# Kernel tuning notes

Measured on AMD Instinct MI355X. Metric: run time of the kernel, lower is better.

Reference implementation:

```python
import jax, jax.numpy as jnp
import numpy as np

D = 1024        # d_hidden
DE = 512        # d_expert (routed)
E = 8           # n_routed_experts
TOP_K = 2
DS = DE * 2     # shared expert width = d_expert * n_shared_experts


def setup_inputs() -> dict:
    key = jax.random.key(0)
    ks = jax.random.split(key, 8)
    s = 1.0 / np.sqrt(D)
    return {
        "x": jax.random.normal(ks[0], (2, 1024, D), dtype=jnp.float32),
        "W_g": jax.random.normal(ks[1], (D, E), dtype=jnp.float32) * s,
        "Wg_e": jax.random.normal(ks[2], (E, D, DE), dtype=jnp.float32) * s,
        "Wu_e": jax.random.normal(ks[3], (E, D, DE), dtype=jnp.float32) * s,
        "Wd_e": jax.random.normal(ks[4], (E, DE, D), dtype=jnp.float32) * (1.0 / np.sqrt(DE)),
        "Wg_s": jax.random.normal(ks[5], (D, DS), dtype=jnp.float32) * s,
        "Wu_s": jax.random.normal(ks[6], (D, DS), dtype=jnp.float32) * s,
        "Wd_s": jax.random.normal(ks[7], (DS, D), dtype=jnp.float32) * (1.0 / np.sqrt(DS)),
    }


def _moe(x, W_g, Wg_e, Wu_e, Wd_e, Wg_s, Wu_s, Wd_s):
    B, T, Dm = x.shape
    N = B * T
    xf = x.reshape(N, Dm)

    # shared expert (SwiGLU)
    shared = (jax.nn.silu(xf @ Wg_s) * (xf @ Wu_s)) @ Wd_s  # [N, D]

    # gating: softmax then top-k (set membership identical to torch sorted=False)
    probs = jax.nn.softmax(xf @ W_g, axis=-1)               # [N, E]
    topk_vals, topk_ids = jax.lax.top_k(probs, TOP_K)       # [N, K]

    # combine weights c[n, e] = sum of topk_vals where routed to expert e
    # (equivalent to the original gather -> weighted scatter_add combine)
    c = jnp.zeros((N, E), dtype=x.dtype)
    c = c.at[jnp.arange(N)[:, None], topk_ids].add(topk_vals)

    # dense per-expert SwiGLU, weighted-combined (same math as gather/scatter loop)
    gate = jax.nn.silu(jnp.einsum('nd,edh->neh', xf, Wg_e))
    up = jnp.einsum('nd,edh->neh', xf, Wu_e)
    routed = jnp.einsum('neh,ne,ehd->nd', gate * up, c, Wd_e)  # [N, D]

    return (shared + routed).reshape(B, T, Dm)


def reference(x, W_g, Wg_e, Wu_e, Wd_e, Wg_s, Wu_s, Wd_s):
    return _moe(x, W_g, Wg_e, Wu_e, Wd_e, Wg_s, Wu_s, Wd_s)
```

## Files before the change

### kernel.cpp

```cpp
#include <hip/hip_runtime.h>
#include <hip/hip_bf16.h>

#define NTOK 2048
#define DIM  1024
#define DEXP 512
#define NEXP 8
#define DSH  1024
#define KH   5120
#define MAXROWS 5120

typedef __hip_bfloat16 bf16;
typedef __attribute__((ext_vector_type(8))) short bf16x8;
typedef __attribute__((ext_vector_type(4))) float floatx4;

__device__ __forceinline__ void gl_lds16(const bf16* g, bf16* l) {
    __builtin_amdgcn_global_load_lds(
        (const __attribute__((address_space(1))) void*)g,
        (__attribute__((address_space(3))) void*)l, 16, 0, 0);
}

__device__ __forceinline__ float b2f(short s) {
    union { float f; unsigned u; } v;
    v.u = ((unsigned)(unsigned short)s) << 16;
    return v.f;
}

__global__ __launch_bounds__(256) void cast_x_kernel(const float* __restrict__ src,
                                                     bf16* __restrict__ dst, int n4) {
    int i = blockIdx.x * 256 + threadIdx.x;
    if (i >= n4) return;
    float4 v = ((const float4*)src)[i];
    struct B4 { bf16 a, b, c, d; };
    B4 o{__float2bfloat16(v.x), __float2bfloat16(v.y),
         __float2bfloat16(v.z), __float2bfloat16(v.w)};
    ((B4*)dst)[i] = o;
}

__global__ __launch_bounds__(256) void pack_weights(
        const float* __restrict__ Wg_s, const float* __restrict__ Wu_s,
        const float* __restrict__ Wg_e, const float* __restrict__ Wu_e,
        const float* __restrict__ Wd_s, const float* __restrict__ Wd_e,
        bf16* __restrict__ Bg, bf16* __restrict__ Bu, bf16* __restrict__ Bd) {
    __shared__ float t[32][33];
    int b = blockIdx.x;
    const float* src; bf16* dst; int C; long dstStride, dstBase; int tilesX;
    if (b < 1024)       { src = Wg_s; dst = Bg; C = 1024; dstStride = 1024; dstBase = 0; tilesX = 32; }
    else if (b < 2048)  { b -= 1024; src = Wu_s; dst = Bu; C = 1024; dstStride = 1024; dstBase = 0; tilesX = 32; }
    else if (b < 6144)  { b -= 2048; int z = b >> 9; b &= 511;
                          src = Wg_e + (long)z * DIM * DEXP; dst = Bg; C = 512;
                          dstStride = 1024; dstBase = (long)(DSH + z * DEXP) * 1024; tilesX = 16; }
    else if (b < 10240) { b -= 6144; int z = b >> 9; b &= 511;
                          src = Wu_e + (long)z * DIM * DEXP; dst = Bu; C = 512;
                          dstStride = 1024; dstBase = (long)(DSH + z * DEXP) * 1024; tilesX = 16; }
    else if (b < 11264) { b -= 10240; src = Wd_s; dst = Bd; C = 1024; dstStride = KH; dstBase = 0; tilesX = 32; }
    else                { b -= 11264; int z = b >> 9; b &= 511;
                          src = Wd_e + (long)z * DEXP * DIM; dst = Bd; C = 1024;
                          dstStride = KH; dstBase = DSH + (long)z * DEXP; tilesX = 32; }
    int tileX = b & (tilesX - 1), tileY = b / tilesX;
    int c0 = tileX * 32, r0 = tileY * 32;
    int tx = threadIdx.x & 31, ty = threadIdx.x >> 5;
#pragma unroll
    for (int i = 0; i < 4; i++)
        t[ty + i * 8][tx] = src[(long)(r0 + ty + i * 8) * C + c0 + tx];
    __syncthreads();
#pragma unroll
    for (int i = 0; i < 4; i++)
        dst[dstBase + (long)(c0 + ty + i * 8) * dstStride + r0 + tx] =
            __float2bfloat16(t[tx][ty + i * 8]);
}

__global__ __launch_bounds__(256) void gate_kernel(const float* __restrict__ x,
                                                   const float* __restrict__ Wg,
                                                   int* __restrict__ counts,
                                                   int* __restrict__ tok_list,
                                                   float* __restrict__ cw,
                                                   int4* __restrict__ tok2slot) {
    int t = blockIdx.x * 4 + (threadIdx.x >> 6);
    int lane = threadIdx.x & 63;
    float acc[NEXP] = {0.f, 0.f, 0.f, 0.f, 0.f, 0.f, 0.f, 0.f};
    const float* xr = x + (long)t * DIM;
    for (int d = lane; d < DIM; d += 64) {
        float xv = xr[d];
        float4 w0 = *(const float4*)(Wg + d * NEXP);
        float4 w1 = *(const float4*)(Wg + d * NEXP + 4);
        acc[0] += xv * w0.x; acc[1] += xv * w0.y; acc[2] += xv * w0.z; acc[3] += xv * w0.w;
        acc[4] += xv * w1.x; acc[5] += xv * w1.y; acc[6] += xv * w1.z; acc[7] += xv * w1.w;
    }
#pragma unroll
    for (int e = 0; e < NEXP; e++)
#pragma unroll
        for (int off = 32; off; off >>= 1)
            acc[e] += __shfl_xor(acc[e], off);
    if (lane == 0) {
        float m = acc[0];
#pragma unroll
        for (int e = 1; e < NEXP; e++) m = fmaxf(m, acc[e]);
        float p[NEXP], s = 0.f;
#pragma unroll
        for (int e = 0; e < NEXP; e++) { p[e] = expf(acc[e] - m); s += p[e]; }
        float inv = 1.f / s;
#pragma unroll
        for (int e = 0; e < NEXP; e++) p[e] *= inv;
        int i1 = 0;
#pragma unroll
        for (int e = 1; e < NEXP; e++) if (p[e] > p[i1]) i1 = e;
        int i2 = (i1 == 0) ? 1 : 0;
#pragma unroll
        for (int e = 0; e < NEXP; e++) if (e != i1 && p[e] > p[i2]) i2 = e;
        int s1 = atomicAdd(counts + i1, 1);
        tok_list[i1 * NTOK + s1] = t;
        cw[i1 * NTOK + s1] = p[i1];
        int s2 = atomicAdd(counts + i2, 1);
        tok_list[i2 * NTOK + s2] = t;
        cw[i2 * NTOK + s2] = p[i2];
        tok2slot[t] = make_int4(i1, s1, i2, s2);
    }
}

__global__ void scan_kernel(const int* __restrict__ counts, int* __restrict__ offs) {
    if (threadIdx.x == 0) {
        int o = 0;
#pragma unroll
        for (int e = 0; e < NEXP; e++) { offs[e] = o; o += (counts[e] + 127) & ~127; }
    }
}

__global__ __launch_bounds__(256) void gu_all(const bf16* __restrict__ X,
                                              const bf16* __restrict__ Bg,
                                              const bf16* __restrict__ Bu,
                                              const int* __restrict__ counts,
                                              const int* __restrict__ offs,
                                              const int* __restrict__ tok_list,
                                              const float* __restrict__ cw,
                                              bf16* __restrict__ Hs,
                                              bf16* __restrict__ He) {
    __shared__ __align__(16) bf16 sA[128 * 32];
    __shared__ __align__(16) bf16 sBg[64 * 32];
    __shared__ __align__(16) bf16 sBu[64 * 32];

    const int b = blockIdx.x;
    const bool routed = b < 1024;
    int e = 0, m, c;
    if (routed) {
        e = b >> 7; m = (b >> 3) & 15; c = b & 7;
        if (m * 128 >= counts[e]) return;
    } else {
        int bs = b - 1024; m = bs >> 4; c = bs & 15;
    }
    const int so = routed ? offs[e] : 0;
    const int colB0 = routed ? (DSH + e * DEXP + c * 64) : c * 64;

    const int tid = threadIdx.x;
    const int wave = tid >> 6, lane = tid & 63;
    const int wr = wave >> 1, wc = wave & 1;
    const int q = lane >> 4, l15 = lane & 15;
    const int koff = (q ^ ((l15 >> 1) & 3)) * 8;

    const int r0 = tid >> 2, c4 = tid & 3;
    const int r1 = r0 + 64;
    const int c4s = c4 ^ ((r0 >> 1) & 3);
    long aRow0, aRow1;
    if (routed) {
        const int* tl = tok_list + e * NTOK + m * 128;
        aRow0 = (long)tl[r0] * DIM;
        aRow1 = (long)tl[r1] * DIM;
    } else {
        aRow0 = (long)(m * 128 + r0) * DIM;
        aRow1 = (long)(m * 128 + r1) * DIM;
    }
    const long bRow = (long)(colB0 + r0) * DIM;

    floatx4 accG[4][2], accU[4][2];
    const floatx4 z4 = {0.f, 0.f, 0.f, 0.f};
#pragma unroll
    for (int i = 0; i < 4; i++)
#pragma unroll
        for (int j = 0; j < 2; j++) { accG[i][j] = z4; accU[i][j] = z4; }

    for (int k0 = 0; k0 < DIM; k0 += 32) {
        gl_lds16(X + aRow0 + k0 + c4s * 8, sA + (wave * 64) * 8);
        gl_lds16(X + aRow1 + k0 + c4s * 8, sA + (256 + wave * 64) * 8);
        gl_lds16(Bg + bRow + k0 + c4s * 8, sBg + (wave * 64) * 8);
        gl_lds16(Bu + bRow + k0 + c4s * 8, sBu + (wave * 64) * 8);
        __syncthreads();

        bf16x8 af[4], bg[2], bu[2];
#pragma unroll
        for (int rt = 0; rt < 4; rt++)
            af[rt] = *(const bf16x8*)(sA + (wr * 64 + rt * 16 + l15) * 32 + koff);
#pragma unroll
        for (int ct = 0; ct < 2; ct++) {
            int cb = (wc * 32 + ct * 16 + l15) * 32 + koff;
            bg[ct] = *(const bf16x8*)(sBg + cb);
            bu[ct] = *(const bf16x8*)(sBu + cb);
        }
#pragma unroll
        for (int rt = 0; rt < 4; rt++)
#pragma unroll
            for (int ct = 0; ct < 2; ct++) {
                accG[rt][ct] = __builtin_amdgcn_mfma_f32_16x16x32_bf16(af[rt], bg[ct], accG[rt][ct], 0, 0, 0);
                accU[rt][ct] = __builtin_amdgcn_mfma_f32_16x16x32_bf16(af[rt], bu[ct], accU[rt][ct], 0, 0, 0);
            }
        __syncthreads();
    }

    float wv[4][4];
#pragma unroll
    for (int rt = 0; rt < 4; rt++)
#pragma unroll
        for (int r = 0; r < 4; r++) {
            int srow = wr * 64 + rt * 16 + q * 4 + r;
            wv[rt][r] = routed ? cw[e * NTOK + m * 128 + srow] : 1.0f;
        }
#pragma unroll
    for (int rt = 0; rt < 4; rt++)
#pragma unroll
        for (int ct = 0; ct < 2; ct++)
#pragma unroll
            for (int r = 0; r < 4; r++) {
                int srow = wr * 64 + rt * 16 + q * 4 + r;
                int colLoc = c * 64 + wc * 32 + ct * 16 + l15;
                float g = accG[rt][ct][r];
                float u = accU[rt][ct][r];
                float h = (g / (1.f + __expf(-g))) * u * wv[rt][r];
                if (routed)
                    He[(long)(so + m * 128 + srow) * DEXP + colLoc] = __float2bfloat16(h);
                else
                    Hs[(long)(m * 128 + srow) * DSH + colLoc] = __float2bfloat16(h);
            }
}

__global__ __launch_bounds__(256) void down_all(const bf16* __restrict__ Hs,
                                                const bf16* __restrict__ He,
                                                const bf16* __restrict__ Bd,
                                                const int* __restrict__ counts,
                                                const int* __restrict__ offs,
                                                bf16* __restrict__ Ys,
                                                bf16* __restrict__ Ye) {
    __shared__ __align__(16) bf16 sA[128 * 32];
    __shared__ __align__(16) bf16 sB[64 * 32];

    const int b = blockIdx.x;
    const bool routed = b < 2048;
    int e = 0, m, cc;
    if (routed) {
        e = b >> 8; m = (b >> 4) & 15; cc = b & 15;
        if (m * 128 >= counts[e]) return;
    } else {
        int bs = b - 2048; m = bs >> 4; cc = bs & 15;
    }
    const int so = routed ? offs[e] : 0;
    const bf16* A = routed ? He + (long)so * DEXP : Hs;
    bf16* Y = routed ? Ye + (long)so * DIM : Ys;
    const int astr = routed ? DEXP : DSH;
    const int ksteps = routed ? (DEXP / 32) : (DSH / 32);
    const int kg0 = routed ? (DSH + e * DEXP) : 0;

    const int tid = threadIdx.x;
    const int wave = tid >> 6, lane = tid & 63;
    const int wr = wave >> 1, wc = wave & 1;
    const int q = lane >> 4, l15 = lane & 15;
    const int koff = (q ^ ((l15 >> 1) & 3)) * 8;

    const int r0 = tid >> 2, c4 = tid & 3;
    const int r1 = r0 + 64;
    const int c4s = c4 ^ ((r0 >> 1) & 3);
    const long aRow0 = (long)(m * 128 + r0) * astr;
    const long aRow1 = (long)(m * 128 + r1) * astr;
    const long bRow = (long)(cc * 64 + r0) * KH + kg0;

    floatx4 acc[4][2];
    const floatx4 z4 = {0.f, 0.f, 0.f, 0.f};
#pragma unroll
    for (int i = 0; i < 4; i++)
#pragma unroll
        for (int j = 0; j < 2; j++) acc[i][j] = z4;

    for (int ks = 0; ks < ksteps; ks++) {
        const int k0 = ks * 32;
        gl_lds16(A + aRow0 + k0 + c4s * 8, sA + (wave * 64) * 8);
        gl_lds16(A + aRow1 + k0 + c4s * 8, sA + (256 + wave * 64) * 8);
        gl_lds16(Bd + bRow + k0 + c4s * 8, sB + (wave * 64) * 8);
        __syncthreads();

        bf16x8 af[4], bb[2];
#pragma unroll
        for (int rt = 0; rt < 4; rt++)
            af[rt] = *(const bf16x8*)(sA + (wr * 64 + rt * 16 + l15) * 32 + koff);
#pragma unroll
        for (int ct = 0; ct < 2; ct++)
            bb[ct] = *(const bf16x8*)(sB + (wc * 32 + ct * 16 + l15) * 32 + koff);
#pragma unroll
        for (int rt = 0; rt < 4; rt++)
#pragma unroll
            for (int ct = 0; ct < 2; ct++)
                acc[rt][ct] = __builtin_amdgcn_mfma_f32_16x16x32_bf16(af[rt], bb[ct], acc[rt][ct], 0, 0, 0);
        __syncthreads();
    }

#pragma unroll
    for (int rt = 0; rt < 4; rt++)
#pragma unroll
        for (int ct = 0; ct < 2; ct++)
#pragma unroll
            for (int r = 0; r < 4; r++) {
                int srow = wr * 64 + rt * 16 + q * 4 + r;
                int mc = cc * 64 + wc * 32 + ct * 16 + l15;
                Y[(long)(m * 128 + srow) * DIM + mc] = __float2bfloat16(acc[rt][ct][r]);
            }
}

__global__ __launch_bounds__(256) void combine_kernel(const bf16* __restrict__ Ys,
                                                      const bf16* __restrict__ Ye,
                                                      const int4* __restrict__ t2s,
                                                      const int* __restrict__ offs,
                                                      float* __restrict__ out) {
    int idx = blockIdx.x * 256 + threadIdx.x;
    int t = idx >> 7;
    int d = (idx & 127) * 8;
    int4 ts = t2s[t];
    bf16x8 a = *(const bf16x8*)(Ys + (long)t * DIM + d);
    bf16x8 p = *(const bf16x8*)(Ye + ((long)offs[ts.x] + ts.y) * DIM + d);
    bf16x8 r = *(const bf16x8*)(Ye + ((long)offs[ts.z] + ts.w) * DIM + d);
    float* o = out + (long)t * DIM + d;
#pragma unroll
    for (int i = 0; i < 8; i++)
        o[i] = b2f(a[i]) + b2f(p[i]) + b2f(r[i]);
}

extern "C" void kernel_launch(void* const* d_in, const int* in_sizes, int n_in,
                              void* d_out, int out_size, void* d_ws, size_t ws_size,
                              hipStream_t stream) {
    const float* x    = (const float*)d_in[0];
    const float* W_g  = (const float*)d_in[1];
    const float* Wg_e = (const float*)d_in[2];
    const float* Wu_e = (const float*)d_in[3];
    const float* Wd_e = (const float*)d_in[4];
    const float* Wd_s_dummy = nullptr; (void)Wd_s_dummy;
    const float* Wg_s = (const float*)d_in[5];
    const float* Wu_s = (const float*)d_in[6];
    const float* Wd_s = (const float*)d_in[7];
    float* out = (float*)d_out;

    bf16* Xb = (bf16*)d_ws;
    bf16* Bg = Xb + (size_t)NTOK * DIM;
    bf16* Bu = Bg + (size_t)KH * DIM;
    bf16* Bd = Bu + (size_t)KH * DIM;
    bf16* Hs = Bd + (size_t)DIM * KH;
    bf16* He = Hs + (size_t)NTOK * DSH;
    bf16* Ys = He + (size_t)MAXROWS * DEXP;
    bf16* Ye = Ys + (size_t)NTOK * DIM;
    int*  counts   = (int*)(Ye + (size_t)MAXROWS * DIM);
    int*  offs     = counts + NEXP;
    int*  tok_list = offs + NEXP;
    float* cw      = (float*)(tok_list + NEXP * NTOK);
    int4* tok2slot = (int4*)(cw + NEXP * NTOK);
    const size_t metaBytes = sizeof(int) * 2 * NEXP
                           + sizeof(int) * NEXP * NTOK + sizeof(float) * NEXP * NTOK;

    hipMemsetAsync(counts, 0, metaBytes, stream);
    cast_x_kernel<<<(NTOK * DIM / 4 + 255) / 256, 256, 0, stream>>>(x, Xb, NTOK * DIM / 4);
    pack_weights<<<15360, 256, 0, stream>>>(Wg_s, Wu_s, Wg_e, Wu_e, Wd_s, Wd_e, Bg, Bu, Bd);
    gate_kernel<<<NTOK / 4, 256, 0, stream>>>(x, W_g, counts, tok_list, cw, tok2slot);
    scan_kernel<<<1, 64, 0, stream>>>(counts, offs);
    gu_all<<<1280, 256, 0, stream>>>(Xb, Bg, Bu, counts, offs, tok_list, cw, Hs, He);
    down_all<<<2304, 256, 0, stream>>>(Hs, He, Bd, counts, offs, Ys, Ye);
    combine_kernel<<<NTOK * DIM / 8 / 256, 256, 0, stream>>>(Ys, Ye, tok2slot, offs, out);
}
```

Before: 238.2 us.

## Fuse x cast into gating, replace atomics with deterministic ballot assignment, vectorize weight pack

The bf16 cast of x now happens inside the gating-logits kernel, so x is read once instead of twice. Slot assignment moves from per-token atomics to a single-block ballot/popcount pass that also computes the padded offsets, which removes the separate scan kernel and makes routing order deterministic. The weight-pack transpose now uses float4 loads and 4-wide bf16 stores with a padded LDS tile. The single-block assign kernel serializes 2048 tokens across 8 waves and adds a launch, though both costs are small.

```diff
diff --git a/kernel.cpp b/kernel.cpp
--- a/kernel.cpp
+++ b/kernel.cpp
@@ -25,15 +25,99 @@
     return v.f;
 }
 
-__global__ __launch_bounds__(256) void cast_x_kernel(const float* __restrict__ src,
-                                                     bf16* __restrict__ dst, int n4) {
-    int i = blockIdx.x * 256 + threadIdx.x;
-    if (i >= n4) return;
-    float4 v = ((const float4*)src)[i];
-    struct B4 { bf16 a, b, c, d; };
-    B4 o{__float2bfloat16(v.x), __float2bfloat16(v.y),
-         __float2bfloat16(v.z), __float2bfloat16(v.w)};
-    ((B4*)dst)[i] = o;
+struct B4 { bf16 a, b, c, d; };
+
+__global__ __launch_bounds__(256) void gate_logits(const float* __restrict__ x,
+                                                   const float* __restrict__ Wg,
+                                                   bf16* __restrict__ Xb,
+                                                   int2* __restrict__ te,
+                                                   float2* __restrict__ tp) {
+    int t = blockIdx.x * 4 + (threadIdx.x >> 6);
+    int lane = threadIdx.x & 63;
+    const float* xr = x + (long)t * DIM;
+    bf16* xo = Xb + (long)t * DIM;
+    float acc[NEXP] = {0.f, 0.f, 0.f, 0.f, 0.f, 0.f, 0.f, 0.f};
+#pragma unroll
+    for (int i = 0; i < 4; i++) {
+        int d = lane * 4 + i * 256;
+        float4 xv = *(const float4*)(xr + d);
+        B4 o{__float2bfloat16(xv.x), __float2bfloat16(xv.y),
+             __float2bfloat16(xv.z), __float2bfloat16(xv.w)};
+        *(B4*)(xo + d) = o;
+#pragma unroll
+        for (int j = 0; j < 4; j++) {
+            float xs = (j == 0) ? xv.x : (j == 1) ? xv.y : (j == 2) ? xv.z : xv.w;
+            float4 w0 = *(const float4*)(Wg + (d + j) * NEXP);
+            float4 w1 = *(const float4*)(Wg + (d + j) * NEXP + 4);
+            acc[0] += xs * w0.x; acc[1] += xs * w0.y; acc[2] += xs * w0.z; acc[3] += xs * w0.w;
+            acc[4] += xs * w1.x; acc[5] += xs * w1.y; acc[6] += xs * w1.z; acc[7] += xs * w1.w;
+        }
+    }
+#pragma unroll
+    for (int e = 0; e < NEXP; e++)
+#pragma unroll
+        for (int off = 32; off; off >>= 1)
+            acc[e] += __shfl_xor(acc[e], off);
+    if (lane == 0) {
+        float m = acc[0];
+#pragma unroll
+        for (int e = 1; e < NEXP; e++) m = fmaxf(m, acc[e]);
+        float p[NEXP], s = 0.f;
+#pragma unroll
+        for (int e = 0; e < NEXP; e++) { p[e] = expf(acc[e] - m); s += p[e]; }
+        float inv = 1.f / s;
+#pragma unroll
+        for (int e = 0; e < NEXP; e++) p[e] *= inv;
+        int i1 = 0;
+#pragma unroll
+        for (int e = 1; e < NEXP; e++) if (p[e] > p[i1]) i1 = e;
+        int i2 = (i1 == 0) ? 1 : 0;
+#pragma unroll
+        for (int e = 0; e < NEXP; e++) if (e != i1 && p[e] > p[i2]) i2 = e;
+        te[t] = make_int2(i1, i2);
+        tp[t] = make_float2(p[i1], p[i2]);
+    }
+}
+
+__global__ __launch_bounds__(512) void assign_kernel(const int2* __restrict__ te,
+                                                     const float2* __restrict__ tp,
+                                                     int* __restrict__ counts,
+                                                     int* __restrict__ offs,
+                                                     int* __restrict__ tok_list,
+                                                     float* __restrict__ cw,
+                                                     int* __restrict__ s1a,
+                                                     int* __restrict__ s2a) {
+    __shared__ int cnt[NEXP];
+    const int e = threadIdx.x >> 6;
+    const int lane = threadIdx.x & 63;
+    int base = 0;
+    for (int t0 = 0; t0 < NTOK; t0 += 64) {
+        int t = t0 + lane;
+        int2 ee = te[t];
+        bool m1 = (ee.x == e), m2 = (ee.y == e);
+        bool mt = m1 || m2;
+        unsigned long long mask = __ballot(mt);
+        int pre = __popcll(mask & ((1ull << lane) - 1ull));
+        if (mt) {
+            int slot = base + pre;
+            tok_list[e * NTOK + slot] = t;
+            float2 pp = tp[t];
+            cw[e * NTOK + slot] = m1 ? pp.x : pp.y;
+            if (m1) s1a[t] = slot; else s2a[t] = slot;
+        }
+        base += __popcll(mask);
+    }
+    if (lane == 0) cnt[e] = base;
+    __syncthreads();
+    if (threadIdx.x == 0) {
+        int o = 0;
+#pragma unroll
+        for (int i = 0; i < NEXP; i++) {
+            counts[i] = cnt[i];
+            offs[i] = o;
+            o += (cnt[i] + 127) & ~127;
+        }
+    }
 }
 
 __global__ __launch_bounds__(256) void pack_weights(
@@ -41,7 +125,7 @@
         const float* __restrict__ Wg_e, const float* __restrict__ Wu_e,
         const float* __restrict__ Wd_s, const float* __restrict__ Wd_e,
         bf16* __restrict__ Bg, bf16* __restrict__ Bu, bf16* __restrict__ Bd) {
-    __shared__ float t[32][33];
+    __shared__ float t[32][36];
     int b = blockIdx.x;
     const float* src; bf16* dst; int C; long dstStride, dstBase; int tilesX;
     if (b < 1024)       { src = Wg_s; dst = Bg; C = 1024; dstStride = 1024; dstBase = 0; tilesX = 32; }
@@ -58,70 +142,19 @@
                           dstStride = KH; dstBase = DSH + (long)z * DEXP; tilesX = 32; }
     int tileX = b & (tilesX - 1), tileY = b / tilesX;
     int c0 = tileX * 32, r0 = tileY * 32;
-    int tx = threadIdx.x & 31, ty = threadIdx.x >> 5;
-#pragma unroll
-    for (int i = 0; i < 4; i++)
-        t[ty + i * 8][tx] = src[(long)(r0 + ty + i * 8) * C + c0 + tx];
+
+    {
+        int row = threadIdx.x >> 3, ch = threadIdx.x & 7;
+        float4 v = *(const float4*)(src + (long)(r0 + row) * C + c0 + ch * 4);
+        *(float4*)(&t[row][ch * 4]) = v;
+    }
     __syncthreads();
-#pragma unroll
-    for (int i = 0; i < 4; i++)
-        dst[dstBase + (long)(c0 + ty + i * 8) * dstStride + r0 + tx] =
-            __float2bfloat16(t[tx][ty + i * 8]);
-}
-
-__global__ __launch_bounds__(256) void gate_kernel(const float* __restrict__ x,
-                                                   const float* __restrict__ Wg,
-                                                   int* __restrict__ counts,
-                                                   int* __restrict__ tok_list,
-                                                   float* __restrict__ cw,
-                                                   int4* __restrict__ tok2slot) {
-    int t = blockIdx.x * 4 + (threadIdx.x >> 6);
-    int lane = threadIdx.x & 63;
-    float acc[NEXP] = {0.f, 0.f, 0.f, 0.f, 0.f, 0.f, 0.f, 0.f};
-    const float* xr = x + (long)t * DIM;
-    for (int d = lane; d < DIM; d += 64) {
-        float xv = xr[d];
-        float4 w0 = *(const float4*)(Wg + d * NEXP);
-        float4 w1 = *(const float4*)(Wg + d * NEXP + 4);
-        acc[0] += xv * w0.x; acc[1] += xv * w0.y; acc[2] += xv * w0.z; acc[3] += xv * w0.w;
-        acc[4] += xv * w1.x; acc[5] += xv * w1.y; acc[6] += xv * w1.z; acc[7] += xv * w1.w;
-    }
-#pragma unroll
-    for (int e = 0; e < NEXP; e++)
-#pragma unroll
-        for (int off = 32; off; off >>= 1)
-            acc[e] += __shfl_xor(acc[e], off);
-    if (lane == 0) {
-        float m = acc[0];
-#pragma unroll
-        for (int e = 1; e < NEXP; e++) m = fmaxf(m, acc[e]);
-        float p[NEXP], s = 0.f;
-#pragma unroll
-        for (int e = 0; e < NEXP; e++) { p[e] = expf(acc[e] - m); s += p[e]; }
-        float inv = 1.f / s;
-#pragma unroll
-        for (int e = 0; e < NEXP; e++) p[e] *= inv;
-        int i1 = 0;
-#pragma unroll
-        for (int e = 1; e < NEXP; e++) if (p[e] > p[i1]) i1 = e;
-        int i2 = (i1 == 0) ? 1 : 0;
-#pragma unroll
-        for (int e = 0; e < NEXP; e++) if (e != i1 && p[e] > p[i2]) i2 = e;
-        int s1 = atomicAdd(counts + i1, 1);
-        tok_list[i1 * NTOK + s1] = t;
-        cw[i1 * NTOK + s1] = p[i1];
-        int s2 = atomicAdd(counts + i2, 1);
-        tok_list[i2 * NTOK + s2] = t;
-        cw[i2 * NTOK + s2] = p[i2];
-        tok2slot[t] = make_int4(i1, s1, i2, s2);
-    }
-}
-
-__global__ void scan_kernel(const int* __restrict__ counts, int* __restrict__ offs) {
-    if (threadIdx.x == 0) {
-        int o = 0;
-#pragma unroll
-        for (int e = 0; e < NEXP; e++) { offs[e] = o; o += (counts[e] + 127) & ~127; }
+    {
+        int dc = threadIdx.x & 31, ch = threadIdx.x >> 5;
+        int j = ch * 4;
+        B4 o{__float2bfloat16(t[j][dc]), __float2bfloat16(t[j + 1][dc]),
+             __float2bfloat16(t[j + 2][dc]), __float2bfloat16(t[j + 3][dc])};
+        *(B4*)(dst + dstBase + (long)(c0 + dc) * dstStride + r0 + j) = o;
     }
 }
 
@@ -312,16 +345,20 @@
 
 __global__ __launch_bounds__(256) void combine_kernel(const bf16* __restrict__ Ys,
                                                       const bf16* __restrict__ Ye,
-                                                      const int4* __restrict__ t2s,
+                                                      const int2* __restrict__ te,
+                                                      const int* __restrict__ s1a,
+                                                      const int* __restrict__ s2a,
                                                       const int* __restrict__ offs,
                                                       float* __restrict__ out) {
     int idx = blockIdx.x * 256 + threadIdx.x;
     int t = idx >> 7;
     int d = (idx & 127) * 8;
-    int4 ts = t2s[t];
+    int2 ee = te[t];
+    long r1 = (long)(offs[ee.x] + s1a[t]);
+    long r2 = (long)(offs[ee.y] + s2a[t]);
     bf16x8 a = *(const bf16x8*)(Ys + (long)t * DIM + d);
-    bf16x8 p = *(const bf16x8*)(Ye + ((long)offs[ts.x] + ts.y) * DIM + d);
-    bf16x8 r = *(const bf16x8*)(Ye + ((long)offs[ts.z] + ts.w) * DIM + d);
+    bf16x8 p = *(const bf16x8*)(Ye + r1 * DIM + d);
+    bf16x8 r = *(const bf16x8*)(Ye + r2 * DIM + d);
     float* o = out + (long)t * DIM + d;
 #pragma unroll
     for (int i = 0; i < 8; i++)
@@ -336,7 +373,6 @@
     const float* Wg_e = (const float*)d_in[2];
     const float* Wu_e = (const float*)d_in[3];
     const float* Wd_e = (const float*)d_in[4];
-    const float* Wd_s_dummy = nullptr; (void)Wd_s_dummy;
     const float* Wg_s = (const float*)d_in[5];
     const float* Wu_s = (const float*)d_in[6];
     const float* Wd_s = (const float*)d_in[7];
@@ -354,16 +390,17 @@
     int*  offs     = counts + NEXP;
     int*  tok_list = offs + NEXP;
     float* cw      = (float*)(tok_list + NEXP * NTOK);
-    int4* tok2slot = (int4*)(cw + NEXP * NTOK);
-    const size_t metaBytes = sizeof(int) * 2 * NEXP
-                           + sizeof(int) * NEXP * NTOK + sizeof(float) * NEXP * NTOK;
-
-    hipMemsetAsync(counts, 0, metaBytes, stream);
-    cast_x_kernel<<<(NTOK * DIM / 4 + 255) / 256, 256, 0, stream>>>(x, Xb, NTOK * DIM / 4);
+    int*  s1a      = (int*)(cw + NEXP * NTOK);
+    int*  s2a      = s1a + NTOK;
+    int2* te       = (int2*)(s2a + NTOK);
+    float2* tp     = (float2*)(te + NTOK);
+
+    hipMemsetAsync(tok_list, 0,
+                   sizeof(int) * NEXP * NTOK + sizeof(float) * NEXP * NTOK, stream);
+    gate_logits<<<NTOK / 4, 256, 0, stream>>>(x, W_g, Xb, te, tp);
+    assign_kernel<<<1, 512, 0, stream>>>(te, tp, counts, offs, tok_list, cw, s1a, s2a);
     pack_weights<<<15360, 256, 0, stream>>>(Wg_s, Wu_s, Wg_e, Wu_e, Wd_s, Wd_e, Bg, Bu, Bd);
-    gate_kernel<<<NTOK / 4, 256, 0, stream>>>(x, W_g, counts, tok_list, cw, tok2slot);
-    scan_kernel<<<1, 64, 0, stream>>>(counts, offs);
     gu_all<<<1280, 256, 0, stream>>>(Xb, Bg, Bu, counts, offs, tok_list, cw, Hs, He);
     down_all<<<2304, 256, 0, stream>>>(Hs, He, Bd, counts, offs, Ys, Ye);
-    combine_kernel<<<NTOK * DIM / 8 / 256, 256, 0, stream>>>(Ys, Ye, tok2slot, offs, out);
-}
+    combine_kernel<<<NTOK * DIM / 8 / 256, 256, 0, stream>>>(Ys, Ye, te, s1a, s2a, offs, out);
+}
```

New measurement: 208.5 us. 12.5% less time.
